# Performance work log

Hardware: AMD Instinct MI355X
Metric: run time of the kernel (lower is better)

Reference implementation:

```python
import jax, jax.numpy as jnp
import numpy as np

NU, NI, E = 20000, 8000, 64
DV, DT = 4096, 768
NE, B = 200000, 4096
L_HET, L_HOMO = 2, 1
K_ISG, K_UCG = 10, 20
MMW, WD = 0.1, 1e-4


def setup_inputs() -> dict:
    ks = jax.random.split(jax.random.key(0), 14)
    return {
        "feat_v": jax.random.normal(ks[0], (NI, DV), jnp.float32),
        "feat_t": jax.random.normal(ks[1], (NI, DT), jnp.float32),
        "pref_v": jax.random.normal(ks[2], (NU, E), jnp.float32) * 0.1,
        "pref_t": jax.random.normal(ks[3], (NU, E), jnp.float32) * 0.1,
        "W_v": jax.random.normal(ks[4], (DV, E), jnp.float32) * 0.02,
        "W_t": jax.random.normal(ks[5], (DT, E), jnp.float32) * 0.02,
        "user_v_alpha": jax.random.normal(ks[6], (1,), jnp.float32),
        "user_nb_weights": jax.random.normal(ks[7], (NU, K_UCG), jnp.float32),
        "edge_users": jax.random.randint(ks[8], (NE,), 0, NU, jnp.int32),
        "edge_items": jax.random.randint(ks[9], (NE,), 0, NI, jnp.int32),
        "u_ids": jax.random.randint(ks[10], (B,), 0, NU, jnp.int32),
        "pos_ids": jax.random.randint(ks[11], (B,), 0, NI, jnp.int32),
        "neg_ids": jax.random.randint(ks[12], (B,), 0, NI, jnp.int32),
        "user_nb": jax.random.randint(ks[13], (NU, K_UCG), 0, NU, jnp.int32),
    }


def reference(feat_v, feat_t, pref_v, pref_t, W_v, W_t, user_v_alpha,
              user_nb_weights, edge_users, edge_items, u_ids, pos_ids,
              neg_ids, user_nb):
    N = NU + NI
    # bidirectional bipartite edges (items offset by NU)
    src = jnp.concatenate([edge_users, edge_items + NU])
    dst = jnp.concatenate([edge_items + NU, edge_users])
    deg = jax.ops.segment_sum(jnp.ones_like(src, jnp.float32), dst, num_segments=N)
    deg = jnp.maximum(deg, 1.0)
    norm = (1.0 / jnp.sqrt(deg[src] * deg[dst]))[:, None]

    def hetero_gcn(feat, pref, W):
        x = jnp.concatenate([pref, feat @ W], axis=0)  # [N, E]
        h, out = x, x
        for _ in range(L_HET):
            h = jax.ops.segment_sum(h[src] * norm, dst, num_segments=N)
            out = out + h
        return out[:NU], out[NU:]

    u_v, i_v = hetero_gcn(feat_v, pref_v, W_v)
    u_t, i_t = hetero_gcn(feat_t, pref_t, W_t)
    a_v = jax.nn.sigmoid(user_v_alpha[0])
    u_f = jnp.concatenate([a_v * u_v, (1.0 - a_v) * u_t], axis=1)  # [NU, 2E]
    i_f = jnp.concatenate([i_v, i_t], axis=1)                      # [NI, 2E]

    # Item Semantic Graph: KNN over cosine sim, no grad through adjacency.
    def knn_adj(f):
        fn = f / jnp.linalg.norm(f, axis=-1, keepdims=True)
        sim = fn @ fn.T                       # [NI, NI]
        _, idx = jax.lax.top_k(sim, K_ISG)
        return jnp.zeros((NI, NI), f.dtype).at[jnp.arange(NI)[:, None], idx].set(1.0)

    adj = jax.lax.stop_gradient(MMW * knn_adj(feat_v) + (1.0 - MMW) * knn_adj(feat_t))
    rs = adj.sum(axis=1)
    adj = adj * jnp.where(rs > 0, 1.0 / rs, 0.0)[:, None]

    h_i = i_f
    for _ in range(L_HOMO):
        h_i = adj @ h_i

    # User Co-occurrence Graph: scatter-softmax attention aggregation, vectorized.
    attn = jax.nn.softmax(user_nb_weights, axis=1)  # [NU, K]
    h_u = u_f
    for _ in range(L_HOMO):
        h_u = jnp.einsum('uk,ukd->ud', attn, h_u[user_nb])

    z_u = u_f + h_u
    z_i = i_f + h_i
    pos = jnp.sum(z_u[u_ids] * z_i[pos_ids], axis=1)
    neg = jnp.sum(z_u[u_ids] * z_i[neg_ids], axis=1)
    bpr = -jnp.mean(jax.nn.log_sigmoid(pos - neg))
    reg = WD * (jnp.sum(pref_v ** 2) + jnp.sum(pref_t ** 2) + user_v_alpha[0] ** 2) / 2.0
    return bpr + reg
```

## Files before the change

kernel.cpp:

```cpp
#include <hip/hip_runtime.h>
#include <cstdint>
#include <cstddef>

#define NU_C   20000
#define NI_C   8000
#define NTOT_C 28000
#define NE_C   200000
#define B_C    4096
#define NPAD_C 8064
#define NCHUNK 63
#define NPAIR  2016

typedef unsigned short u16;
typedef unsigned int   u32;
typedef unsigned char  u8;
typedef __bf16 bf16x8 __attribute__((ext_vector_type(8)));
typedef float  f32x4  __attribute__((ext_vector_type(4)));

static __device__ __forceinline__ u16 f2bf(float f) {
  u32 u = __float_as_uint(f);
  return (u16)((u + 0x7fffu + ((u >> 16) & 1u)) >> 16);
}

static __device__ __forceinline__ void gl_lds16(const void* g, void* l) {
  __builtin_amdgcn_global_load_lds(
      (const __attribute__((address_space(1))) void*)g,
      (__attribute__((address_space(3))) void*)l, 16, 0, 0);
}

__global__ void conv_kernel2(const float* __restrict__ Fv, const float* __restrict__ Ft,
                             u16* __restrict__ Fbv, u16* __restrict__ Fbt,
                             u8* __restrict__ Fv8,
                             float* __restrict__ rnv, float* __restrict__ rnt) {
  int b = blockIdx.x;
  const int tid = threadIdx.x;
  float ss = 0.f;
  if (b < NPAD_C) {
    const int row = b;
    u16* dst  = Fbv + (size_t)row * 4096;
    u8*  dst8 = Fv8 + (size_t)row * 4096;
    if (row < NI_C) {
      const float* src = Fv + (size_t)row * 4096;
      for (int c = tid * 4; c < 4096; c += 1024) {
        float4 f = *(const float4*)(src + c);
        ss += f.x*f.x + f.y*f.y + f.z*f.z + f.w*f.w;
        ushort4 v; v.x = f2bf(f.x); v.y = f2bf(f.y); v.z = f2bf(f.z); v.w = f2bf(f.w);
        *(ushort4*)(dst + c) = v;
        int w8 = __builtin_amdgcn_cvt_pk_fp8_f32(f.x, f.y, 0, false);
        w8 = __builtin_amdgcn_cvt_pk_fp8_f32(f.z, f.w, w8, true);
        *(u32*)(dst8 + c) = (u32)w8;
      }
    } else {
      for (int c = tid * 4; c < 4096; c += 1024) {
        ushort4 v; v.x = v.y = v.z = v.w = 0;
        *(ushort4*)(dst + c) = v;
        *(u32*)(dst8 + c) = 0u;
      }
    }
    #pragma unroll
    for (int off = 32; off; off >>= 1) ss += __shfl_xor(ss, off);
    __shared__ float red[4];
    if ((tid & 63) == 0) red[tid >> 6] = ss;
    __syncthreads();
    if (tid == 0) {
      float s = red[0] + red[1] + red[2] + red[3];
      rnv[row] = (row < NI_C) ? rsqrtf(s) : 0.f;
    }
  } else {
    const int row = b - NPAD_C;
    u16* dst = Fbt + (size_t)row * 768;
    if (row < NI_C) {
      const float* src = Ft + (size_t)row * 768;
      for (int c = tid * 4; c < 768; c += 1024) {
        float4 f = *(const float4*)(src + c);
        ss += f.x*f.x + f.y*f.y + f.z*f.z + f.w*f.w;
        ushort4 v; v.x = f2bf(f.x); v.y = f2bf(f.y); v.z = f2bf(f.z); v.w = f2bf(f.w);
        *(ushort4*)(dst + c) = v;
      }
    } else {
      for (int c = tid * 4; c < 768; c += 1024) {
        ushort4 v; v.x = v.y = v.z = v.w = 0;
        *(ushort4*)(dst + c) = v;
      }
    }
    #pragma unroll
    for (int off = 32; off; off >>= 1) ss += __shfl_xor(ss, off);
    __shared__ float red[4];
    if ((tid & 63) == 0) red[tid >> 6] = ss;
    __syncthreads();
    if (tid == 0) {
      float s = red[0] + red[1] + red[2] + red[3];
      rnt[row] = (row < NI_C) ? rsqrtf(s) : 0.f;
    }
  }
}

__launch_bounds__(256)
__global__ void simtopk_sym_fp8_kernel(const u8* __restrict__ F, const float* __restrict__ rn,
                                       u32* __restrict__ tv) {
  __shared__ __align__(16) char smem[34816];
  u8*    sB   = (u8*)smem;
  u8*    sA   = (u8*)(smem + 16384);
  float* T    = (float*)smem;
  int*   mk   = (int*)smem;
  int*   mk2  = (int*)(smem + 20480);
  float* sRNI = (float*)(smem + 33792);
  float* sRNJ = (float*)(smem + 34304);

  const int tid  = threadIdx.x;
  const int lane = tid & 63;
  const int wv   = tid >> 6;
  const int n15  = lane & 15;
  const int quad = lane >> 4;

  int I = 0, rem = blockIdx.x;
  { int rowlen = NCHUNK;
    while (rem >= rowlen) { rem -= rowlen; rowlen--; I++; } }
  const int J = I + rem;

  const int l2   = lane >> 2;
  const int lseg = (lane & 3) ^ (l2 & 3) ^ (lane >> 4);
  const u8* gB[2]; const u8* gA[2]; u8* lB[2]; u8* lA[2];
  #pragma unroll
  for (int rep = 0; rep < 2; ++rep) {
    int row = wv * 32 + rep * 16 + l2;
    gB[rep] = F + (size_t)(I * 128 + row) * 4096 + lseg * 16;
    gA[rep] = F + (size_t)(J * 128 + row) * 4096 + lseg * 16;
    lB[rep] = sB + (wv * 32 + rep * 16) * 64;
    lA[rep] = sA + (wv * 32 + rep * 16) * 64;
  }
  const int s_n = (n15 & 3) ^ (n15 >> 2);
  const int q2  = quad >> 1;
  const int q8  = (quad & 1) * 8;
  const int rB0 = (wv * 32 + n15) * 64;
  const int rB1 = rB0 + 16 * 64;

  f32x4 acc[2][8];
  #pragma unroll
  for (int tf = 0; tf < 2; ++tf)
    #pragma unroll
    for (int af = 0; af < 8; ++af) { f32x4 z = {0.f,0.f,0.f,0.f}; acc[tf][af] = z; }

  for (int k0 = 0; k0 < 4096; k0 += 128) {
    __syncthreads();
    gl_lds16(gB[0] + k0,      lB[0]);
    gl_lds16(gB[0] + k0 + 64, lB[0] + 8192);
    gl_lds16(gB[1] + k0,      lB[1]);
    gl_lds16(gB[1] + k0 + 64, lB[1] + 8192);
    gl_lds16(gA[0] + k0,      lA[0]);
    gl_lds16(gA[0] + k0 + 64, lA[0] + 8192);
    gl_lds16(gA[1] + k0,      lA[1]);
    gl_lds16(gA[1] + k0 + 64, lA[1] + 8192);
    if (k0 == 0) {
      if (tid < 128) sRNJ[tid] = rn[J * 128 + tid];
      else           sRNI[tid - 128] = rn[I * 128 + (tid - 128)];
    }
    __syncthreads();
    #pragma unroll
    for (int ksub = 0; ksub < 2; ++ksub) {
      const u8* bBase = sB + ksub * 8192;
      const u8* aBase = sA + ksub * 8192;
      #pragma unroll
      for (int ks = 0; ks < 2; ++ks) {
        const int sw = (((ks * 2 + q2) ^ s_n) << 4) + q8;
        long long b0 = *(const long long*)(bBase + rB0 + sw);
        long long b1 = *(const long long*)(bBase + rB1 + sw);
        #pragma unroll
        for (int af = 0; af < 8; ++af) {
          long long a = *(const long long*)(aBase + (af * 16 + n15) * 64 + sw);
          acc[0][af] = __builtin_amdgcn_mfma_f32_16x16x32_fp8_fp8(a, b0, acc[0][af], 0, 0, 0);
          acc[1][af] = __builtin_amdgcn_mfma_f32_16x16x32_fp8_fp8(a, b1, acc[1][af], 0, 0, 0);
        }
      }
    }
  }

  int bk[2][10];
  #pragma unroll
  for (int tf = 0; tf < 2; ++tf)
    #pragma unroll
    for (int j = 0; j < 10; ++j) bk[tf][j] = 0;

  #pragma unroll
  for (int af = 0; af < 8; ++af) {
    const float4 rn4 = *(const float4*)(sRNJ + af * 16 + quad * 4);
    const float rna[4] = {rn4.x, rn4.y, rn4.z, rn4.w};
    #pragma unroll
    for (int r = 0; r < 4; ++r) {
      const int ci = J * 128 + af * 16 + quad * 4 + r;
      #pragma unroll
      for (int tf = 0; tf < 2; ++tf) {
        float v = acc[tf][af][r] * rna[r];
        int key = (int)((__float_as_uint(v) & 0xFFFFE000u) | (u32)ci);
        if (ci < NI_C && key > bk[tf][9]) {
          bk[tf][9] = key;
          #pragma unroll
          for (int j = 9; j > 0; --j)
            if (bk[tf][j] > bk[tf][j-1]) { int t = bk[tf][j]; bk[tf][j] = bk[tf][j-1]; bk[tf][j-1] = t; }
        }
      }
    }
  }
  __syncthreads();
  #pragma unroll
  for (int tf = 0; tf < 2; ++tf) {
    int rl = wv * 32 + tf * 16 + n15;
    #pragma unroll
    for (int j = 0; j < 10; ++j) mk[rl * 40 + quad * 10 + j] = bk[tf][j];
  }
  __syncthreads();
  if (tid < 128) {
    int* m = mk + tid * 40;
    int h0 = 0, h1 = 10, h2 = 20, h3 = 30;
    int v0 = m[0], v1 = m[10], v2 = m[20], v3 = m[30];
    #pragma unroll
    for (int s = 0; s < 10; ++s) {
      int m01 = v0 > v1 ? v0 : v1, m23 = v2 > v3 ? v2 : v3;
      int mx = m01 > m23 ? m01 : m23;
      mk2[tid * 10 + s] = mx;
      if      (mx == v0) { ++h0; v0 = (h0 < 10) ? m[h0] : (int)0x80000000; }
      else if (mx == v1) { ++h1; v1 = (h1 < 20) ? m[h1] : (int)0x80000000; }
      else if (mx == v2) { ++h2; v2 = (h2 < 30) ? m[h2] : (int)0x80000000; }
      else               { ++h3; v3 = (h3 < 40) ? m[h3] : (int)0x80000000; }
    }
  }
  __syncthreads();
  { u32* o = tv + ((size_t)J * NPAD_C + I * 128) * 10;
    for (int g = tid; g < 1280; g += 256) o[g] = (u32)mk2[g]; }

  if (I == J) return;

  int bj[2][10];
  #pragma unroll
  for (int s = 0; s < 2; ++s)
    #pragma unroll
    for (int j = 0; j < 10; ++j) bj[s][j] = 0;

  #pragma unroll
  for (int tf = 0; tf < 2; ++tf) {
    __syncthreads();
    #pragma unroll
    for (int af = 0; af < 8; ++af)
      #pragma unroll
      for (int r = 0; r < 4; ++r)
        T[(af * 16 + quad * 4 + r) * 66 + wv * 16 + n15] = acc[tf][af][r];
    __syncthreads();
    #pragma unroll
    for (int s = 0; s < 2; ++s) {
      const int c_own = wv * 32 + s * 16 + n15;
      #pragma unroll
      for (int j = 0; j < 16; ++j) {
        const int t  = quad * 32 + tf * 16 + j;
        const int t64 = quad * 16 + j;
        float v = T[c_own * 66 + t64] * sRNI[t];
        const int ti = I * 128 + t;
        int key = (int)((__float_as_uint(v) & 0xFFFFE000u) | (u32)ti);
        if (ti < NI_C && key > bj[s][9]) {
          bj[s][9] = key;
          #pragma unroll
          for (int q = 9; q > 0; --q)
            if (bj[s][q] > bj[s][q-1]) { int tt = bj[s][q]; bj[s][q] = bj[s][q-1]; bj[s][q-1] = tt; }
        }
      }
    }
  }
  __syncthreads();
  #pragma unroll
  for (int s = 0; s < 2; ++s) {
    int rl = wv * 32 + s * 16 + n15;
    #pragma unroll
    for (int j = 0; j < 10; ++j) mk[rl * 40 + quad * 10 + j] = bj[s][j];
  }
  __syncthreads();
  if (tid < 128) {
    int* m = mk + tid * 40;
    int h0 = 0, h1 = 10, h2 = 20, h3 = 30;
    int v0 = m[0], v1 = m[10], v2 = m[20], v3 = m[30];
    #pragma unroll
    for (int s = 0; s < 10; ++s) {
      int m01 = v0 > v1 ? v0 : v1, m23 = v2 > v3 ? v2 : v3;
      int mx = m01 > m23 ? m01 : m23;
      mk2[tid * 10 + s] = mx;
      if      (mx == v0) { ++h0; v0 = (h0 < 10) ? m[h0] : (int)0x80000000; }
      else if (mx == v1) { ++h1; v1 = (h1 < 20) ? m[h1] : (int)0x80000000; }
      else if (mx == v2) { ++h2; v2 = (h2 < 30) ? m[h2] : (int)0x80000000; }
      else               { ++h3; v3 = (h3 < 40) ? m[h3] : (int)0x80000000; }
    }
  }
  __syncthreads();
  { u32* o = tv + ((size_t)I * NPAD_C + J * 128) * 10;
    for (int g = tid; g < 1280; g += 256) o[g] = (u32)mk2[g]; }
}

template<int D>
__launch_bounds__(256)
__global__ void simtopk_sym_kernel(const u16* __restrict__ F, const float* __restrict__ rn,
                                   u32* __restrict__ tv) {
  __shared__ __align__(16) char smem[40960];
  u16*   sB   = (u16*)smem;
  u16*   sA   = (u16*)(smem + 16384);
  float* T    = (float*)smem;
  int*   mk   = (int*)smem;
  int*   mk2  = (int*)(smem + 20480);
  float* sRNI = (float*)(smem + 34816);
  float* sRNJ = (float*)(smem + 35328);

  const int tid  = threadIdx.x;
  const int lane = tid & 63;
  const int wv   = tid >> 6;
  const int n15  = lane & 15;
  const int quad = lane >> 4;

  int I = 0, rem = blockIdx.x;
  { int rowlen = NCHUNK;
    while (rem >= rowlen) { rem -= rowlen; rowlen--; I++; } }
  const int J = I + rem;

  const int l8  = lane >> 3;
  const int sgu = ((lane & 7) ^ l8) << 3;
  const u16* gB[4]; const u16* gA[4]; u16* lB[4]; u16* lA[4];
  #pragma unroll
  for (int rep = 0; rep < 4; ++rep) {
    int row = wv * 32 + rep * 8 + l8;
    gB[rep] = F + (size_t)(I * 128 + row) * D + sgu;
    gA[rep] = F + (size_t)(J * 128 + row) * D + sgu;
    lB[rep] = sB + wv * 2048 + rep * 512;
    lA[rep] = sA + wv * 2048 + rep * 512;
  }
  const int swu0 = ((quad    ) ^ (n15 & 7)) << 3;
  const int swu1 = ((quad + 4) ^ (n15 & 7)) << 3;
  const int rowB0 = (wv * 32 + n15) * 64;
  const int rowB1 = rowB0 + 16 * 64;

  f32x4 acc[2][8];
  #pragma unroll
  for (int tf = 0; tf < 2; ++tf)
    #pragma unroll
    for (int af = 0; af < 8; ++af) { f32x4 z = {0.f,0.f,0.f,0.f}; acc[tf][af] = z; }

  for (int k0 = 0; k0 < D; k0 += 64) {
    __syncthreads();
    #pragma unroll
    for (int rep = 0; rep < 4; ++rep) gl_lds16(gB[rep] + k0, lB[rep]);
    #pragma unroll
    for (int rep = 0; rep < 4; ++rep) gl_lds16(gA[rep] + k0, lA[rep]);
    if (k0 == 0) {
      if (tid < 128) sRNJ[tid] = rn[J * 128 + tid];
      else           sRNI[tid - 128] = rn[I * 128 + (tid - 128)];
    }
    __syncthreads();
    #pragma unroll
    for (int ks = 0; ks < 2; ++ks) {
      const int swu = ks ? swu1 : swu0;
      bf16x8 b0 = *(const bf16x8*)(sB + rowB0 + swu);
      bf16x8 b1 = *(const bf16x8*)(sB + rowB1 + swu);
      #pragma unroll
      for (int af = 0; af < 8; ++af) {
        bf16x8 a = *(const bf16x8*)(sA + (af * 16 + n15) * 64 + swu);
        acc[0][af] = __builtin_amdgcn_mfma_f32_16x16x32_bf16(a, b0, acc[0][af], 0, 0, 0);
        acc[1][af] = __builtin_amdgcn_mfma_f32_16x16x32_bf16(a, b1, acc[1][af], 0, 0, 0);
      }
    }
  }

  int bk[2][10];
  #pragma unroll
  for (int tf = 0; tf < 2; ++tf)
    #pragma unroll
    for (int j = 0; j < 10; ++j) bk[tf][j] = 0;

  #pragma unroll
  for (int af = 0; af < 8; ++af) {
    const float4 rn4 = *(const float4*)(sRNJ + af * 16 + quad * 4);
    const float rna[4] = {rn4.x, rn4.y, rn4.z, rn4.w};
    #pragma unroll
    for (int r = 0; r < 4; ++r) {
      const int ci = J * 128 + af * 16 + quad * 4 + r;
      #pragma unroll
      for (int tf = 0; tf < 2; ++tf) {
        float v = acc[tf][af][r] * rna[r];
        int key = (int)((__float_as_uint(v) & 0xFFFFE000u) | (u32)ci);
        if (ci < NI_C && key > bk[tf][9]) {
          bk[tf][9] = key;
          #pragma unroll
          for (int j = 9; j > 0; --j)
            if (bk[tf][j] > bk[tf][j-1]) { int t = bk[tf][j]; bk[tf][j] = bk[tf][j-1]; bk[tf][j-1] = t; }
        }
      }
    }
  }
  __syncthreads();
  #pragma unroll
  for (int tf = 0; tf < 2; ++tf) {
    int rl = wv * 32 + tf * 16 + n15;
    #pragma unroll
    for (int j = 0; j < 10; ++j) mk[rl * 40 + quad * 10 + j] = bk[tf][j];
  }
  __syncthreads();
  if (tid < 128) {
    int* m = mk + tid * 40;
    int h0 = 0, h1 = 10, h2 = 20, h3 = 30;
    int v0 = m[0], v1 = m[10], v2 = m[20], v3 = m[30];
    #pragma unroll
    for (int s = 0; s < 10; ++s) {
      int m01 = v0 > v1 ? v0 : v1, m23 = v2 > v3 ? v2 : v3;
      int mx = m01 > m23 ? m01 : m23;
      mk2[tid * 10 + s] = mx;
      if      (mx == v0) { ++h0; v0 = (h0 < 10) ? m[h0] : (int)0x80000000; }
      else if (mx == v1) { ++h1; v1 = (h1 < 20) ? m[h1] : (int)0x80000000; }
      else if (mx == v2) { ++h2; v2 = (h2 < 30) ? m[h2] : (int)0x80000000; }
      else               { ++h3; v3 = (h3 < 40) ? m[h3] : (int)0x80000000; }
    }
  }
  __syncthreads();
  { u32* o = tv + ((size_t)J * NPAD_C + I * 128) * 10;
    for (int g = tid; g < 1280; g += 256) o[g] = (u32)mk2[g]; }

  if (I == J) return;

  int bj[2][10];
  #pragma unroll
  for (int s = 0; s < 2; ++s)
    #pragma unroll
    for (int j = 0; j < 10; ++j) bj[s][j] = 0;

  #pragma unroll
  for (int tf = 0; tf < 2; ++tf) {
    __syncthreads();
    #pragma unroll
    for (int af = 0; af < 8; ++af)
      #pragma unroll
      for (int r = 0; r < 4; ++r)
        T[(af * 16 + quad * 4 + r) * 66 + wv * 16 + n15] = acc[tf][af][r];
    __syncthreads();
    #pragma unroll
    for (int s = 0; s < 2; ++s) {
      const int c_own = wv * 32 + s * 16 + n15;
      #pragma unroll
      for (int j = 0; j < 16; ++j) {
        const int t  = quad * 32 + tf * 16 + j;
        const int t64 = quad * 16 + j;
        float v = T[c_own * 66 + t64] * sRNI[t];
        const int ti = I * 128 + t;
        int key = (int)((__float_as_uint(v) & 0xFFFFE000u) | (u32)ti);
        if (ti < NI_C && key > bj[s][9]) {
          bj[s][9] = key;
          #pragma unroll
          for (int q = 9; q > 0; --q)
            if (bj[s][q] > bj[s][q-1]) { int tt = bj[s][q]; bj[s][q] = bj[s][q-1]; bj[s][q-1] = tt; }
        }
      }
    }
  }
  __syncthreads();
  #pragma unroll
  for (int s = 0; s < 2; ++s) {
    int rl = wv * 32 + s * 16 + n15;
    #pragma unroll
    for (int j = 0; j < 10; ++j) mk[rl * 40 + quad * 10 + j] = bj[s][j];
  }
  __syncthreads();
  if (tid < 128) {
    int* m = mk + tid * 40;
    int h0 = 0, h1 = 10, h2 = 20, h3 = 30;
    int v0 = m[0], v1 = m[10], v2 = m[20], v3 = m[30];
    #pragma unroll
    for (int s = 0; s < 10; ++s) {
      int m01 = v0 > v1 ? v0 : v1, m23 = v2 > v3 ? v2 : v3;
      int mx = m01 > m23 ? m01 : m23;
      mk2[tid * 10 + s] = mx;
      if      (mx == v0) { ++h0; v0 = (h0 < 10) ? m[h0] : (int)0x80000000; }
      else if (mx == v1) { ++h1; v1 = (h1 < 20) ? m[h1] : (int)0x80000000; }
      else if (mx == v2) { ++h2; v2 = (h2 < 30) ? m[h2] : (int)0x80000000; }
      else               { ++h3; v3 = (h3 < 40) ? m[h3] : (int)0x80000000; }
    }
  }
  __syncthreads();
  { u32* o = tv + ((size_t)I * NPAD_C + J * 128) * 10;
    for (int g = tid; g < 1280; g += 256) o[g] = (u32)mk2[g]; }
}

__global__ void merge_topk_kernel(const u32* __restrict__ tv, int* __restrict__ idx) {
  __shared__ int fk[640];
  const int row = blockIdx.x;
  const int tid = threadIdx.x;
  for (int g = tid; g < 630; g += 64)
    fk[g] = (int)tv[((size_t)(g / 10) * NPAD_C + row) * 10 + (g % 10)];
  if (tid < 10) fk[630 + tid] = (int)0x80000000;
  __syncthreads();
  int v[10];
  #pragma unroll
  for (int j = 0; j < 10; ++j) v[j] = fk[tid + j * 64];
  #pragma unroll 1
  for (int s = 0; s < 10; ++s) {
    int loc = v[0];
    #pragma unroll
    for (int j = 1; j < 10; ++j) loc = v[j] > loc ? v[j] : loc;
    #pragma unroll
    for (int off = 32; off; off >>= 1) {
      int o = __shfl_xor(loc, off); loc = o > loc ? o : loc;
    }
    if (tid == 0) idx[row * 10 + s] = loc & 0x1FFF;
    #pragma unroll
    for (int j = 0; j < 10; ++j) if (v[j] == loc) v[j] = (int)0x80000000;
  }
}

__global__ void deg_count_kernel(const int* __restrict__ eu, const int* __restrict__ ei,
                                 float* deg) {
  int e = blockIdx.x * 256 + threadIdx.x;
  if (e < NE_C) {
    atomicAdd(&deg[eu[e]], 1.f);
    atomicAdd(&deg[NU_C + ei[e]], 1.f);
  }
}

__global__ void scan_kernel(float* __restrict__ deg, int* __restrict__ row_start,
                            int* __restrict__ cursor) {
  __shared__ int part[1024];
  const int tid = threadIdx.x;
  const int base = tid * 28;
  float dl[28];
  int local[28];
  int s = 0;
  #pragma unroll
  for (int j = 0; j < 28; ++j) {
    int n = base + j;
    float df = (n < NTOT_C) ? deg[n] : 0.f;
    dl[j] = df;
    local[j] = s; s += (int)df;
  }
  part[tid] = s;
  __syncthreads();
  for (int off = 1; off < 1024; off <<= 1) {
    int v = (tid >= off) ? part[tid - off] : 0;
    __syncthreads();
    part[tid] += v;
    __syncthreads();
  }
  int pre = (tid > 0) ? part[tid - 1] : 0;
  #pragma unroll
  for (int j = 0; j < 28; ++j) {
    int n = base + j;
    if (n < NTOT_C) {
      row_start[n] = pre + local[j];
      cursor[n]    = pre + local[j];
      deg[n]       = rsqrtf(fmaxf(dl[j], 1.f));
    }
  }
  if (tid == 1023) row_start[NTOT_C] = part[1023];
}

__global__ void place_kernel(const int* __restrict__ eu, const int* __restrict__ ei,
                             const float* __restrict__ dinv, int* __restrict__ cursor,
                             int* __restrict__ esrc, float* __restrict__ ew) {
  int e = blockIdx.x * 256 + threadIdx.x;
  if (e >= NE_C) return;
  int u = eu[e], v = NU_C + ei[e];
  float w = dinv[u] * dinv[v];
  int p1 = atomicAdd(&cursor[v], 1);  esrc[p1] = u; ew[p1] = w;
  int p2 = atomicAdd(&cursor[u], 1);  esrc[p2] = v; ew[p2] = w;
}

__global__ void wtrans_kernel(const float* __restrict__ Wv, const float* __restrict__ Wti,
                              u16* __restrict__ Ov, u16* __restrict__ Ot) {
  __shared__ u16 sT[64][72];
  int b = blockIdx.x;
  const float* W; u16* O; int D;
  if (b < 64) { W = Wv; O = Ov; D = 4096; }
  else        { b -= 64; W = Wti; O = Ot; D = 768; }
  const int k0 = b * 64;
  const int r = threadIdx.x >> 6;
  const int c = threadIdx.x & 63;
  for (int rr = r; rr < 64; rr += 4)
    sT[c][rr] = f2bf(W[(size_t)(k0 + rr) * 64 + c]);
  __syncthreads();
  const int n = threadIdx.x >> 2, seg = threadIdx.x & 3;
  uint4 a0 = *(const uint4*)&sT[n][seg * 16];
  uint4 a1 = *(const uint4*)&sT[n][seg * 16 + 8];
  *(uint4*)(O + (size_t)n * D + k0 + seg * 16)     = a0;
  *(uint4*)(O + (size_t)n * D + k0 + seg * 16 + 8) = a1;
}

template<int D>
__launch_bounds__(256)
__global__ void gemm_xw_kernel(const u16* __restrict__ F, const u16* __restrict__ Wt,
                               float* __restrict__ x2, int modeoff) {
  __shared__ __align__(16) u16 sF[64 * 64];
  const int tid  = threadIdx.x;
  const int lane = tid & 63;
  const int wv   = tid >> 6;
  const int n15  = lane & 15;
  const int quad = lane >> 4;
  const int l8   = lane >> 3;
  const int sgu  = ((lane & 7) ^ l8) << 3;
  const u16* gF[2]; u16* lF[2];
  #pragma unroll
  for (int rep = 0; rep < 2; ++rep) {
    int row = rep * 32 + wv * 8 + l8;
    gF[rep] = F + (size_t)(blockIdx.x * 64 + row) * D + sgu;
    lF[rep] = sF + (rep * 32 + wv * 8) * 64;
  }
  const int swu0 = ((quad    ) ^ (n15 & 7)) << 3;
  const int swu1 = ((quad + 4) ^ (n15 & 7)) << 3;

  f32x4 acc[4];
  #pragma unroll
  for (int nf = 0; nf < 4; ++nf) { f32x4 z = {0.f,0.f,0.f,0.f}; acc[nf] = z; }

  for (int k0 = 0; k0 < D; k0 += 64) {
    __syncthreads();
    gl_lds16(gF[0] + k0, lF[0]);
    gl_lds16(gF[1] + k0, lF[1]);
    __syncthreads();
    #pragma unroll
    for (int ks = 0; ks < 2; ++ks) {
      const int swu = ks ? swu1 : swu0;
      bf16x8 a = *(const bf16x8*)(sF + (wv * 16 + n15) * 64 + swu);
      #pragma unroll
      for (int nf = 0; nf < 4; ++nf) {
        bf16x8 b = *(const bf16x8*)(Wt + (size_t)(nf * 16 + n15) * D + k0 + ks * 32 + quad * 8);
        acc[nf] = __builtin_amdgcn_mfma_f32_16x16x32_bf16(a, b, acc[nf], 0, 0, 0);
      }
    }
  }
  #pragma unroll
  for (int nf = 0; nf < 4; ++nf)
    #pragma unroll
    for (int r = 0; r < 4; ++r) {
      int row = blockIdx.x * 64 + wv * 16 + quad * 4 + r;
      if (row < NI_C)
        x2[(size_t)(NU_C + row) * 128 + modeoff + nf * 16 + n15] = acc[nf][r];
    }
}

__global__ void fill_pref_kernel(const float* __restrict__ pv, const float* __restrict__ pt,
                                 float* __restrict__ x2) {
  int gid = blockIdx.x * 256 + threadIdx.x;
  int u = gid >> 7, c = gid & 127;
  x2[gid] = (c < 64) ? pv[(size_t)u * 64 + c] : pt[(size_t)u * 64 + (c - 64)];
}

__global__ void gather2_kernel(const int* __restrict__ row_start, const int* __restrict__ esrc,
                               const float* __restrict__ ew, const float* __restrict__ x2,
                               float* __restrict__ h1) {
  const int node = blockIdx.x * 2 + (threadIdx.x >> 7);
  const int ch   = threadIdx.x & 127;
  if (node >= NTOT_C) return;
  const int b = row_start[node], e = row_start[node + 1];
  float acc = 0.f;
  for (int i = b; i < e; ++i)
    acc += ew[i] * x2[(size_t)esrc[i] * 128 + ch];
  h1[(size_t)node * 128 + ch] = acc;
}

__global__ void gather_comb2_kernel(const int* __restrict__ row_start, const int* __restrict__ esrc,
                                    const float* __restrict__ ew, const float* __restrict__ x2,
                                    const float* __restrict__ h1, const float* __restrict__ alpha,
                                    float* __restrict__ uf, float* __restrict__ ifb) {
  const int node = blockIdx.x * 2 + (threadIdx.x >> 7);
  const int ch   = threadIdx.x & 127;
  if (node >= NTOT_C) return;
  const int b = row_start[node], e = row_start[node + 1];
  float acc = 0.f;
  for (int i = b; i < e; ++i)
    acc += ew[i] * h1[(size_t)esrc[i] * 128 + ch];
  float val = x2[(size_t)node * 128 + ch] + h1[(size_t)node * 128 + ch] + acc;
  if (node < NU_C) {
    float av = 1.f / (1.f + expf(-alpha[0]));
    float coef = (ch < 64) ? av : (1.f - av);
    uf[(size_t)node * 128 + ch] = coef * val;
  } else {
    ifb[(size_t)(node - NU_C) * 128 + ch] = val;
  }
}

__global__ void zuzi_kernel(const float* __restrict__ uf, const float* __restrict__ w,
                            const int* __restrict__ nb, const float* __restrict__ ifb,
                            const int* __restrict__ iv, const int* __restrict__ it,
                            float* __restrict__ zu, float* __restrict__ zi) {
  const int c = threadIdx.x;
  if (blockIdx.x < NU_C) {
    const int u = blockIdx.x;
    __shared__ float at[20];
    if (c < 20) at[c] = w[u * 20 + c];
    __syncthreads();
    float e[20]; float m = -1e30f;
    #pragma unroll
    for (int k = 0; k < 20; ++k) { e[k] = at[k]; m = fmaxf(m, e[k]); }
    float ssum = 0.f;
    #pragma unroll
    for (int k = 0; k < 20; ++k) { e[k] = expf(e[k] - m); ssum += e[k]; }
    float inv = 1.f / ssum;
    float acc = 0.f;
    #pragma unroll
    for (int k = 0; k < 20; ++k) {
      int j = nb[u * 20 + k];
      acc += e[k] * inv * uf[(size_t)j * 128 + c];
    }
    zu[(size_t)u * 128 + c] = uf[(size_t)u * 128 + c] + acc;
  } else {
    const int i = blockIdx.x - NU_C;
    float sv = 0.f, st = 0.f;
    #pragma unroll
    for (int k = 0; k < 10; ++k) sv += ifb[(size_t)iv[i * 10 + k] * 128 + c];
    #pragma unroll
    for (int k = 0; k < 10; ++k) st += ifb[(size_t)it[i * 10 + k] * 128 + c];
    zi[(size_t)i * 128 + c] = ifb[(size_t)i * 128 + c] + 0.01f * sv + 0.09f * st;
  }
}

__global__ void loss_kernel(const float* __restrict__ zu, const float* __restrict__ zi,
                            const int* __restrict__ uid, const int* __restrict__ pid,
                            const int* __restrict__ nid, const float* __restrict__ pv,
                            const float* __restrict__ pt, const float* __restrict__ alpha,
                            float* __restrict__ out) {
  if (blockIdx.x < 1024) {
    int wv = threadIdx.x >> 6, lane = threadIdx.x & 63;
    int b = blockIdx.x * 4 + wv;
    int u = uid[b], p = pid[b], n = nid[b];
    float2 a  = *(const float2*)(zu + (size_t)u * 128 + lane * 2);
    float2 xp = *(const float2*)(zi + (size_t)p * 128 + lane * 2);
    float2 xn = *(const float2*)(zi + (size_t)n * 128 + lane * 2);
    float d = a.x * (xp.x - xn.x) + a.y * (xp.y - xn.y);
    #pragma unroll
    for (int off = 32; off; off >>= 1) d += __shfl_xor(d, off);
    if (lane == 0) {
      float xv = -d;
      float sp = fmaxf(xv, 0.f) + log1pf(expf(-fabsf(xv)));
      atomicAdd(out, sp * (1.f / (float)B_C));
    }
  } else {
    const size_t N1 = (size_t)NU_C * 64;
    float acc = 0.f;
    for (size_t i = (size_t)(blockIdx.x - 1024) * 256 + threadIdx.x; i < 2 * N1;
         i += (size_t)512 * 256) {
      float x = (i < N1) ? pv[i] : pt[i - N1];
      acc += x * x;
    }
    #pragma unroll
    for (int off = 32; off; off >>= 1) acc += __shfl_xor(acc, off);
    __shared__ float red[4];
    if ((threadIdx.x & 63) == 0) red[threadIdx.x >> 6] = acc;
    __syncthreads();
    if (threadIdx.x == 0) {
      float s = red[0] + red[1] + red[2] + red[3];
      atomicAdd(out, 0.5e-4f * s);
    }
    if (blockIdx.x == 1024 && threadIdx.x == 0) {
      float a = alpha[0];
      atomicAdd(out, 0.5e-4f * a * a);
    }
  }
}

extern "C" void kernel_launch(void* const* d_in, const int* in_sizes, int n_in,
                              void* d_out, int out_size, void* d_ws, size_t ws_size,
                              hipStream_t stream) {
  const float* feat_v = (const float*)d_in[0];
  const float* feat_t = (const float*)d_in[1];
  const float* pref_v = (const float*)d_in[2];
  const float* pref_t = (const float*)d_in[3];
  const float* W_v    = (const float*)d_in[4];
  const float* W_t    = (const float*)d_in[5];
  const float* alpha  = (const float*)d_in[6];
  const float* unw    = (const float*)d_in[7];
  const int* eu       = (const int*)d_in[8];
  const int* ei       = (const int*)d_in[9];
  const int* u_ids    = (const int*)d_in[10];
  const int* pos_ids  = (const int*)d_in[11];
  const int* neg_ids  = (const int*)d_in[12];
  const int* user_nb  = (const int*)d_in[13];
  float* out = (float*)d_out;
  char* ws = (char*)d_ws;

  size_t off = 0;
  auto alloc = [&](size_t bytes) { char* p = ws + off; off += (bytes + 255) & ~(size_t)255; return p; };
  u16*   fvbf  = (u16*)alloc((size_t)NPAD_C * 4096 * 2);
  u8*    fv8   = (u8*)alloc((size_t)NPAD_C * 4096);
  u16*   ftbf  = (u16*)alloc((size_t)NPAD_C * 768 * 2);
  u16*   wtv   = (u16*)alloc((size_t)64 * 4096 * 2);
  u16*   wtt   = (u16*)alloc((size_t)64 * 768 * 2);
  float* rn_v  = (float*)alloc(NPAD_C * 4);
  float* rn_t  = (float*)alloc(NPAD_C * 4);
  int*   idx_v = (int*)alloc(NI_C * 10 * 4);
  int*   idx_t = (int*)alloc(NI_C * 10 * 4);
  float* dinv  = (float*)alloc(NTOT_C * 4);
  int*   rowst = (int*)alloc((NTOT_C + 1) * 4);
  int*   curs  = (int*)alloc(NTOT_C * 4);
  int*   esrc  = (int*)alloc((size_t)2 * NE_C * 4);
  float* ew    = (float*)alloc((size_t)2 * NE_C * 4);
  float* x2    = (float*)alloc((size_t)NTOT_C * 128 * 4);
  float* h1    = (float*)alloc((size_t)NTOT_C * 128 * 4);
  char*  pC    = alloc((size_t)(NU_C + NI_C) * 128 * 4 * 2);
  u32*   tvb   = (u32*)pC;
  float* u_f   = (float*)pC;
  float* i_f   = (float*)(pC + (size_t)NU_C * 128 * 4);
  float* z_u   = (float*)(pC + (size_t)(NU_C + NI_C) * 128 * 4);
  float* z_i   = (float*)(pC + (size_t)(2 * NU_C + NI_C) * 128 * 4);

  hipMemsetAsync(out, 0, sizeof(float), stream);
  hipMemsetAsync(dinv, 0, NTOT_C * 4, stream);

  deg_count_kernel<<<(NE_C + 255) / 256, 256, 0, stream>>>(eu, ei, dinv);
  scan_kernel<<<1, 1024, 0, stream>>>(dinv, rowst, curs);
  place_kernel<<<(NE_C + 255) / 256, 256, 0, stream>>>(eu, ei, dinv, curs, esrc, ew);

  conv_kernel2<<<2 * NPAD_C, 256, 0, stream>>>(feat_v, feat_t, fvbf, ftbf, fv8, rn_v, rn_t);
  wtrans_kernel<<<76, 256, 0, stream>>>(W_v, W_t, wtv, wtt);

  simtopk_sym_fp8_kernel<<<NPAIR, 256, 0, stream>>>(fv8, rn_v, tvb);
  merge_topk_kernel<<<NI_C, 64, 0, stream>>>(tvb, idx_v);
  simtopk_sym_kernel<768><<<NPAIR, 256, 0, stream>>>(ftbf, rn_t, tvb);
  merge_topk_kernel<<<NI_C, 64, 0, stream>>>(tvb, idx_t);

  fill_pref_kernel<<<(NU_C * 128) / 256, 256, 0, stream>>>(pref_v, pref_t, x2);
  gemm_xw_kernel<4096><<<125, 256, 0, stream>>>(fvbf, wtv, x2, 0);
  gemm_xw_kernel<768><<<125, 256, 0, stream>>>(ftbf, wtt, x2, 64);
  gather2_kernel<<<14000, 256, 0, stream>>>(rowst, esrc, ew, x2, h1);
  gather_comb2_kernel<<<14000, 256, 0, stream>>>(rowst, esrc, ew, x2, h1, alpha, u_f, i_f);

  zuzi_kernel<<<NU_C + NI_C, 128, 0, stream>>>(u_f, unw, user_nb, i_f, idx_v, idx_t, z_u, z_i);
  loss_kernel<<<1536, 256, 0, stream>>>(z_u, z_i, u_ids, pos_ids, neg_ids,
                                        pref_v, pref_t, alpha, out);
}
```

Measured before the change: 1.096 ms.

## Double-buffer LDS tiles in fp8 similarity top-k kernel

Splits the k-loop into stage and compute phases over two LDS buffers, so global-to-LDS loads for the next 128-wide k slice are issued while MFMAs consume the current slice. This removes one barrier per slice and aims to hide memory latency behind compute. The cost is roughly double the shared memory per block, which may reduce how many blocks fit on each CU.

```diff
diff --git a/kernel.cpp b/kernel.cpp
--- a/kernel.cpp
+++ b/kernel.cpp
@@ -98,14 +98,12 @@
 __launch_bounds__(256)
 __global__ void simtopk_sym_fp8_kernel(const u8* __restrict__ F, const float* __restrict__ rn,
                                        u32* __restrict__ tv) {
-  __shared__ __align__(16) char smem[34816];
-  u8*    sB   = (u8*)smem;
-  u8*    sA   = (u8*)(smem + 16384);
+  __shared__ __align__(16) char smem[66560];
   float* T    = (float*)smem;
   int*   mk   = (int*)smem;
   int*   mk2  = (int*)(smem + 20480);
-  float* sRNI = (float*)(smem + 33792);
-  float* sRNJ = (float*)(smem + 34304);
+  float* sRNI = (float*)(smem + 65536);
+  float* sRNJ = (float*)(smem + 66048);
 
   const int tid  = threadIdx.x;
   const int lane = tid & 63;
@@ -120,14 +118,14 @@
 
   const int l2   = lane >> 2;
   const int lseg = (lane & 3) ^ (l2 & 3) ^ (lane >> 4);
-  const u8* gB[2]; const u8* gA[2]; u8* lB[2]; u8* lA[2];
+  const u8* gB[2]; const u8* gA[2];
+  int lo[2];
   #pragma unroll
   for (int rep = 0; rep < 2; ++rep) {
     int row = wv * 32 + rep * 16 + l2;
     gB[rep] = F + (size_t)(I * 128 + row) * 4096 + lseg * 16;
     gA[rep] = F + (size_t)(J * 128 + row) * 4096 + lseg * 16;
-    lB[rep] = sB + (wv * 32 + rep * 16) * 64;
-    lA[rep] = sA + (wv * 32 + rep * 16) * 64;
+    lo[rep] = (wv * 32 + rep * 16) * 64;
   }
   const int s_n = (n15 & 3) ^ (n15 >> 2);
   const int q2  = quad >> 1;
@@ -141,25 +139,20 @@
     #pragma unroll
     for (int af = 0; af < 8; ++af) { f32x4 z = {0.f,0.f,0.f,0.f}; acc[tf][af] = z; }
 
-  for (int k0 = 0; k0 < 4096; k0 += 128) {
-    __syncthreads();
-    gl_lds16(gB[0] + k0,      lB[0]);
-    gl_lds16(gB[0] + k0 + 64, lB[0] + 8192);
-    gl_lds16(gB[1] + k0,      lB[1]);
-    gl_lds16(gB[1] + k0 + 64, lB[1] + 8192);
-    gl_lds16(gA[0] + k0,      lA[0]);
-    gl_lds16(gA[0] + k0 + 64, lA[0] + 8192);
-    gl_lds16(gA[1] + k0,      lA[1]);
-    gl_lds16(gA[1] + k0 + 64, lA[1] + 8192);
-    if (k0 == 0) {
-      if (tid < 128) sRNJ[tid] = rn[J * 128 + tid];
-      else           sRNI[tid - 128] = rn[I * 128 + (tid - 128)];
-    }
-    __syncthreads();
+  auto stage = [&](char* buf, int k0) {
+    #pragma unroll
+    for (int rep = 0; rep < 2; ++rep) {
+      gl_lds16(gB[rep] + k0,      buf + lo[rep]);
+      gl_lds16(gB[rep] + k0 + 64, buf + 8192 + lo[rep]);
+      gl_lds16(gA[rep] + k0,      buf + 16384 + lo[rep]);
+      gl_lds16(gA[rep] + k0 + 64, buf + 24576 + lo[rep]);
+    }
+  };
+  auto compute = [&](const char* buf) {
     #pragma unroll
     for (int ksub = 0; ksub < 2; ++ksub) {
-      const u8* bBase = sB + ksub * 8192;
-      const u8* aBase = sA + ksub * 8192;
+      const u8* bBase = (const u8*)buf + ksub * 8192;
+      const u8* aBase = (const u8*)buf + 16384 + ksub * 8192;
       #pragma unroll
       for (int ks = 0; ks < 2; ++ks) {
         const int sw = (((ks * 2 + q2) ^ s_n) << 4) + q8;
@@ -173,6 +166,20 @@
         }
       }
     }
+  };
+
+  if (tid < 128) sRNJ[tid] = rn[J * 128 + tid];
+  else           sRNI[tid - 128] = rn[I * 128 + (tid - 128)];
+  stage(smem, 0);
+  __syncthreads();
+
+  for (int k0 = 0; k0 < 4096; k0 += 256) {
+    stage(smem + 32768, k0 + 128);
+    compute(smem);
+    __syncthreads();
+    if (k0 + 256 < 4096) stage(smem, k0 + 256);
+    compute(smem + 32768);
+    __syncthreads();
   }
 
   int bk[2][10];
```

New measurement: 1.103 ms. No clear change (+0.6%).
